# Performance work log

Measured on AMD Instinct MI355X. Metric: run time of the kernel, lower is better.

## Reference

```python
import jax, jax.numpy as jnp
import numpy as np
from jax import lax

R = 3
D = (2 * R + 1) ** 2  # 49 local offsets


def _unfold(x, r):
    # torch F.unfold(kernel=2r+1, padding=r): (B,C,H,W) -> (B, C*K*K, H, W),
    # channel-major (c, ky, kx) ordering, matching conv_general_dilated_patches.
    k = 2 * r + 1
    return lax.conv_general_dilated_patches(
        x, (k, k), (1, 1), [(r, r), (r, r)],
        dimension_numbers=("NCHW", "OIHW", "NCHW"))


def _l2norm(x, eps=1e-12):
    n = jnp.sqrt(jnp.sum(x * x, axis=1, keepdims=True))
    return x / jnp.maximum(n, eps)


def setup_inputs() -> dict:
    key = jax.random.key(0)
    ks = jax.random.split(key, 8)
    B, Cin, Cmid, H, W = 2, 256, 128, 112, 112
    phi_cur = jax.random.normal(ks[0], (B, Cin, H, W), jnp.float32)
    phi_rnd = jax.random.normal(ks[1], (B, Cin, H, W), jnp.float32)
    P_cur = jax.random.normal(ks[2], (B, 3, H, W), jnp.float32)
    P_rnd = jax.random.normal(ks[3], (B, 3, H, W), jnp.float32)
    Wq = jax.random.normal(ks[4], (Cmid, Cin), jnp.float32) * 0.05
    Wk = jax.random.normal(ks[5], (Cmid, Cin), jnp.float32) * 0.05
    Wv = jax.random.normal(ks[6], (D, D), jnp.float32) * 0.1
    bv = jnp.zeros((D,), jnp.float32)
    gamma = jnp.array(1.0, jnp.float32)
    return dict(phi_cur=phi_cur, phi_rnd=phi_rnd, P_cur=P_cur, P_rnd=P_rnd,
                Wq=Wq, Wk=Wk, Wv=Wv, bv=bv, gamma=gamma)


def reference(phi_cur, phi_rnd, P_cur, P_rnd, Wq, Wk, Wv, bv, gamma):
    B, _, H, W = phi_cur.shape
    # 1x1 convs + channel L2 normalize
    q = _l2norm(jnp.einsum('oc,bchw->bohw', Wq, phi_cur))
    k = _l2norm(jnp.einsum('oc,bchw->bohw', Wk, phi_rnd))
    # local cost volume: patches (B, Cmid, D, H, W)
    patches = _unfold(k, R).reshape(B, -1, D, H, W)
    corr = jnp.einsum('bchw,bcdhw->bdhw', q, patches)  # (B,D,H,W)
    vol_corr = jnp.einsum('ed,bdhw->behw', Wv, corr) + bv[None, :, None, None]
    # geometric bias
    Pr = _unfold(P_rnd, R).reshape(B, 3, D, H, W)
    dP = P_cur[:, :, None, :, :] - Pr  # (B,3,D,H,W)
    dz = dP[:, 2]
    dist = jnp.sqrt(jnp.clip(jnp.sum(dP * dP, axis=1), 1e-12, None))
    logits = vol_corr + gamma * (-dist - 0.5 * jnp.abs(dz))
    w = jax.nn.softmax(logits, axis=1)
    off = jnp.arange(-R, R + 1, dtype=w.dtype)
    dY, dX = jnp.meshgrid(off, off, indexing='ij')
    offx = dX.reshape(1, D, 1, 1)
    offy = dY.reshape(1, D, 1, 1)
    du = jnp.sum(w * offx, axis=1, keepdims=True)
    dv = jnp.sum(w * offy, axis=1, keepdims=True)
    conf = jnp.max(w, axis=1, keepdims=True)
    return du, dv, conf
```

## Files before the change

kernel.cpp:

```cpp
#include <hip/hip_runtime.h>
#include <hip/hip_bf16.h>
#include <math.h>

constexpr int B    = 2;
constexpr int CIN  = 256;
constexpr int CMID = 128;
constexpr int H    = 112;
constexpr int W    = 112;
constexpr int HW   = H * W;
constexpr int NPIX = B * HW;
constexpr int RAD  = 3;
constexpr int KS   = 7;
constexpr int DD   = 49;

typedef __attribute__((ext_vector_type(8))) short  short8;
typedef __attribute__((ext_vector_type(4))) float  float4v;

__device__ __forceinline__ unsigned pkbf(float a, float b) {
    union { __hip_bfloat162 h; unsigned u; } c;
    c.h = __float22bfloat162_rn(make_float2(a, b));
    return c.u;
}

constexpr int PSTR = 264;

__global__ __launch_bounds__(256) void proj_mfma(
    const float* __restrict__ phi_cur, const float* __restrict__ phi_rnd,
    const float* __restrict__ Wq, const float* __restrict__ Wk,
    unsigned short* __restrict__ q_ws, unsigned short* __restrict__ k_ws)
{
    __shared__ unsigned short pt[64 * PSTR];
    __shared__ float red[4][64];

    const int tid  = threadIdx.x;
    const int lane = tid & 63;
    const int wv   = __builtin_amdgcn_readfirstlane(tid >> 6);
    const int t    = blockIdx.y;

    const float* __restrict__ phi = t ? phi_rnd : phi_cur;
    const float* __restrict__ Wm  = t ? Wk : Wq;
    unsigned short* __restrict__ outp = t ? k_ws : q_ws;

    const int pgb = blockIdx.x * 64;
    const int b   = pgb / HW;
    const int pim = pgb % HW;
    const float* pbase = phi + (size_t)b * CIN * HW + pim;

#pragma unroll
    for (int pass = 0; pass < 8; ++pass) {
        const int idx = pass * 256 + tid;
        const int cp  = idx >> 4;
        const int pq  = idx & 15;
        const int c0  = cp * 2;
        const float4 va = *(const float4*)(pbase + (size_t)c0 * HW + pq * 4);
        const float4 vb = *(const float4*)(pbase + (size_t)(c0 + 1) * HW + pq * 4);
        *(unsigned*)(pt + (pq * 4 + 0) * PSTR + c0) = pkbf(va.x, vb.x);
        *(unsigned*)(pt + (pq * 4 + 1) * PSTR + c0) = pkbf(va.y, vb.y);
        *(unsigned*)(pt + (pq * 4 + 2) * PSTR + c0) = pkbf(va.z, vb.z);
        *(unsigned*)(pt + (pq * 4 + 3) * PSTR + c0) = pkbf(va.w, vb.w);
    }

    const int m = lane & 15, quad = lane >> 4;
    short8 af[2][8];
#pragma unroll
    for (int ot = 0; ot < 2; ++ot)
#pragma unroll
        for (int kc = 0; kc < 8; ++kc) {
            const float* wr = Wm + (size_t)(wv * 32 + ot * 16 + m) * CIN
                                 + kc * 32 + quad * 8;
            const float4 w0 = *(const float4*)(wr);
            const float4 w1 = *(const float4*)(wr + 4);
            union { short8 s; unsigned u[4]; } pk;
            pk.u[0] = pkbf(w0.x, w0.y);
            pk.u[1] = pkbf(w0.z, w0.w);
            pk.u[2] = pkbf(w1.x, w1.y);
            pk.u[3] = pkbf(w1.z, w1.w);
            af[ot][kc] = pk.s;
        }

    __syncthreads();

    float4v acc[2][4];
#pragma unroll
    for (int ot = 0; ot < 2; ++ot)
#pragma unroll
        for (int nt = 0; nt < 4; ++nt) acc[ot][nt] = (float4v)0.f;

#pragma unroll
    for (int kc = 0; kc < 8; ++kc) {
        short8 bf[4];
#pragma unroll
        for (int nt = 0; nt < 4; ++nt)
            bf[nt] = *(const short8*)(pt + (nt * 16 + m) * PSTR + kc * 32 + quad * 8);
#pragma unroll
        for (int ot = 0; ot < 2; ++ot)
#pragma unroll
            for (int nt = 0; nt < 4; ++nt)
                acc[ot][nt] = __builtin_amdgcn_mfma_f32_16x16x32_bf16(
                    af[ot][kc], bf[nt], acc[ot][nt], 0, 0, 0);
    }

#pragma unroll
    for (int nt = 0; nt < 4; ++nt) {
        float ss = 0.f;
#pragma unroll
        for (int ot = 0; ot < 2; ++ot)
#pragma unroll
            for (int r = 0; r < 4; ++r)
                ss = fmaf(acc[ot][nt][r], acc[ot][nt][r], ss);
        ss += __shfl_xor(ss, 16, 64);
        ss += __shfl_xor(ss, 32, 64);
        if (quad == 0) red[wv][nt * 16 + m] = ss;
    }
    __syncthreads();

    float inv[4];
#pragma unroll
    for (int nt = 0; nt < 4; ++nt) {
        const int px = nt * 16 + m;
        const float tot = red[0][px] + red[1][px] + red[2][px] + red[3][px];
        inv[nt] = 1.f / fmaxf(sqrtf(tot), 1e-12f);
    }

#pragma unroll
    for (int nt = 0; nt < 4; ++nt)
#pragma unroll
        for (int ot = 0; ot < 2; ++ot) {
            uint2 st;
            st.x = pkbf(acc[ot][nt][0] * inv[nt], acc[ot][nt][1] * inv[nt]);
            st.y = pkbf(acc[ot][nt][2] * inv[nt], acc[ot][nt][3] * inv[nt]);
            *(uint2*)(outp + (size_t)(pgb + nt * 16 + m) * CMID
                      + wv * 32 + ot * 16 + quad * 4) = st;
        }
}

constexpr int TILE = 16;
constexpr int COLS = TILE + 6;
constexpr int NV   = KS * COLS;

__global__ __launch_bounds__(256, 4) void corr_kernel(
    const unsigned short* __restrict__ q_ws, const unsigned short* __restrict__ k_ws,
    const float* __restrict__ P_cur, const float* __restrict__ P_rnd,
    const float* __restrict__ Wvm, const float* __restrict__ bv,
    const float* __restrict__ gamma_p, float* __restrict__ out)
{
    __shared__ float cs[TILE][52];
    __shared__ float prt[3 * NV];

    const int tid  = threadIdx.x;
    const int lane = tid & 63;
    const int wv   = __builtin_amdgcn_readfirstlane(tid >> 6);
    const int w0   = blockIdx.x * TILE;
    const int h    = blockIdx.y;
    const int b    = blockIdx.z;

#pragma unroll
    for (int pass = 0; pass < 2; ++pass) {
        const int idx = pass * 256 + tid;
        if (idx < 3 * NV) {
            const int ch = idx / NV;
            const int vi = idx % NV;
            const int rr = vi / COLS;
            const int cc = vi % COLS;
            const int hh = h + rr - RAD;
            const int ww = w0 + cc - RAD;
            float v = 0.f;
            if (hh >= 0 && hh < H && ww >= 0 && ww < W)
                v = P_rnd[((size_t)b * 3 + ch) * HW + hh * W + ww];
            prt[idx] = v;
        }
    }

    if (tid < TILE * 3)
        cs[tid / 3][49 + tid % 3] = 0.f;

    const int  ld    = (lane < DD) ? lane : 0;
    const bool valid = (lane < DD);
    float wrow[52];
#pragma unroll
    for (int e = 0; e < DD; ++e) wrow[e] = Wvm[ld * DD + e];
    wrow[49] = wrow[50] = wrow[51] = 0.f;
    const float bvv   = bv[ld];
    const float gamma = gamma_p[0];

    const int m = lane & 15, quad = lane >> 4;
    const unsigned short* qbase =
        q_ws + (size_t)(b * HW + h * W + w0 + m) * CMID + quad * 8;

    for (int g = wv; g < 14; g += 4) {
        const int r  = g >> 1;
        const int nt = g & 1;
        const int hh = h + r - RAD;
        const int ww = w0 + nt * 16 + m - RAD;
        const bool inb = (hh >= 0) && (hh < H) && (ww >= 0) && (ww < W);
        const unsigned short* kbase =
            k_ws + (size_t)(b * HW + hh * W + ww) * CMID + quad * 8;

        float4v acc = (float4v)0.f;
#pragma unroll
        for (int kc = 0; kc < 4; ++kc) {
            const short8 afrag = *(const short8*)(qbase + kc * 32);
            const short8 bfrag = inb ? *(const short8*)(kbase + kc * 32)
                                     : (short8)0;
            acc = __builtin_amdgcn_mfma_f32_16x16x32_bf16(afrag, bfrag, acc, 0, 0, 0);
        }
#pragma unroll
        for (int reg = 0; reg < 4; ++reg) {
            const int p   = quad * 4 + reg;
            const int off = nt * 16 + m - p;
            if (off >= 0 && off <= 6)
                cs[p][r * 7 + off] = acc[reg];
        }
    }
    __syncthreads();

    const int dyr = ld / KS;
    const int dxc = ld % KS;
    const int dy  = dyr - RAD;
    const int dx  = dxc - RAD;
    const float fdx = (float)dx, fdy = (float)dy;

    for (int i = 0; i < 4; ++i) {
        const int pl = wv * 4 + i;
        const int pg = b * HW + h * W + w0 + pl;

        const int vi = dyr * COLS + pl + dxc;
        const float rx = prt[vi];
        const float ry = prt[NV + vi];
        const float rz = prt[2 * NV + vi];
        const float* pc = P_cur + (size_t)b * 3 * HW + (h * W + w0 + pl);
        const float cx = pc[0], cy = pc[HW], cz = pc[2 * HW];
        const float dpx = cx - rx, dpy = cy - ry, dpz = cz - rz;
        const float dist = sqrtf(fmaxf(dpx * dpx + dpy * dpy + dpz * dpz, 1e-12f));

        float logit = -INFINITY;
        if (valid) {
            float v = bvv;
#pragma unroll
            for (int e4 = 0; e4 < 13; ++e4) {
                const float4 c4 = *(const float4*)&cs[pl][e4 * 4];
                v = fmaf(wrow[e4 * 4 + 0], c4.x, v);
                v = fmaf(wrow[e4 * 4 + 1], c4.y, v);
                v = fmaf(wrow[e4 * 4 + 2], c4.z, v);
                v = fmaf(wrow[e4 * 4 + 3], c4.w, v);
            }
            logit = v + gamma * (-dist - 0.5f * fabsf(dpz));
        }

        float lmax = logit;
#pragma unroll
        for (int off = 32; off; off >>= 1)
            lmax = fmaxf(lmax, __shfl_xor(lmax, off, 64));
        const float e1 = valid ? __expf(logit - lmax) : 0.f;

        float s0 = e1, s1 = e1 * fdx, s2 = e1 * fdy;
#pragma unroll
        for (int off = 32; off; off >>= 1) {
            s0 += __shfl_xor(s0, off, 64);
            s1 += __shfl_xor(s1, off, 64);
            s2 += __shfl_xor(s2, off, 64);
        }

        if (lane == 0) {
            const float rZ = 1.f / s0;
            out[pg]            = s1 * rZ;
            out[NPIX + pg]     = s2 * rZ;
            out[2 * NPIX + pg] = rZ;
        }
    }
}

extern "C" void kernel_launch(void* const* d_in, const int* in_sizes, int n_in,
                              void* d_out, int out_size, void* d_ws, size_t ws_size,
                              hipStream_t stream)
{
    const float* phi_cur = (const float*)d_in[0];
    const float* phi_rnd = (const float*)d_in[1];
    const float* P_cur   = (const float*)d_in[2];
    const float* P_rnd   = (const float*)d_in[3];
    const float* Wq      = (const float*)d_in[4];
    const float* Wk      = (const float*)d_in[5];
    const float* Wv      = (const float*)d_in[6];
    const float* bv      = (const float*)d_in[7];
    const float* gm      = (const float*)d_in[8];
    float* out = (float*)d_out;

    unsigned short* ws   = (unsigned short*)d_ws;
    unsigned short* q_ws = ws;
    unsigned short* k_ws = q_ws + (size_t)NPIX * CMID;

    proj_mfma<<<dim3(NPIX / 64, 2), 256, 0, stream>>>(
        phi_cur, phi_rnd, Wq, Wk, q_ws, k_ws);

    corr_kernel<<<dim3(W / TILE, H, B), 256, 0, stream>>>(
        q_ws, k_ws, P_cur, P_rnd, Wv, bv, gm, out);
}
```

Before: 148.0 us.

## Map one pixel per lane with online softmax over a 4x16 tile

The correlation kernel now handles a 4x16 pixel tile per block, so grid blocks drop fourfold and the P_rnd halo is shared across four rows. In the epilogue each lane owns one pixel: it loads all 49 correlations into registers and loops over offsets with an online softmax. Wv rows are read as wave-uniform scalar loads, which removes the cross-lane shuffle reductions and the idle lanes 49-63. The cost is a serial 49x49 FMA loop per lane plus two exps per offset, and higher register pressure from the 49-element array.

```diff
diff --git a/kernel.cpp b/kernel.cpp
--- a/kernel.cpp
+++ b/kernel.cpp
@@ -134,9 +134,12 @@
         }
 }
 
-constexpr int TILE = 16;
-constexpr int COLS = TILE + 6;
-constexpr int NV   = KS * COLS;
+constexpr int BH   = 4;
+constexpr int BW   = 16;
+constexpr int PRH  = BH + 6;
+constexpr int PRW  = BW + 6;
+constexpr int PRN  = PRH * PRW;
+constexpr int CSTR = 53;
 
 __global__ __launch_bounds__(256, 4) void corr_kernel(
     const unsigned short* __restrict__ q_ws, const unsigned short* __restrict__ k_ws,
@@ -144,25 +147,25 @@
     const float* __restrict__ Wvm, const float* __restrict__ bv,
     const float* __restrict__ gamma_p, float* __restrict__ out)
 {
-    __shared__ float cs[TILE][52];
-    __shared__ float prt[3 * NV];
+    __shared__ float cs[64 * CSTR];
+    __shared__ float prt[3 * PRN];
 
     const int tid  = threadIdx.x;
     const int lane = tid & 63;
     const int wv   = __builtin_amdgcn_readfirstlane(tid >> 6);
-    const int w0   = blockIdx.x * TILE;
-    const int h    = blockIdx.y;
+    const int w0   = blockIdx.x * BW;
+    const int h0   = blockIdx.y * BH;
     const int b    = blockIdx.z;
 
 #pragma unroll
-    for (int pass = 0; pass < 2; ++pass) {
+    for (int pass = 0; pass < 3; ++pass) {
         const int idx = pass * 256 + tid;
-        if (idx < 3 * NV) {
-            const int ch = idx / NV;
-            const int vi = idx % NV;
-            const int rr = vi / COLS;
-            const int cc = vi % COLS;
-            const int hh = h + rr - RAD;
+        if (idx < 3 * PRN) {
+            const int ch = idx / PRN;
+            const int sl = idx % PRN;
+            const int rr = sl / PRW;
+            const int cc = sl % PRW;
+            const int hh = h0 + rr - RAD;
             const int ww = w0 + cc - RAD;
             float v = 0.f;
             if (hh >= 0 && hh < H && ww >= 0 && ww < W)
@@ -171,28 +174,17 @@
         }
     }
 
-    if (tid < TILE * 3)
-        cs[tid / 3][49 + tid % 3] = 0.f;
-
-    const int  ld    = (lane < DD) ? lane : 0;
-    const bool valid = (lane < DD);
-    float wrow[52];
-#pragma unroll
-    for (int e = 0; e < DD; ++e) wrow[e] = Wvm[ld * DD + e];
-    wrow[49] = wrow[50] = wrow[51] = 0.f;
-    const float bvv   = bv[ld];
-    const float gamma = gamma_p[0];
-
     const int m = lane & 15, quad = lane >> 4;
-    const unsigned short* qbase =
-        q_ws + (size_t)(b * HW + h * W + w0 + m) * CMID + quad * 8;
-
-    for (int g = wv; g < 14; g += 4) {
-        const int r  = g >> 1;
-        const int nt = g & 1;
-        const int hh = h + r - RAD;
+    for (int g = wv; g < 56; g += 4) {
+        const int hq = g / 14;
+        const int rem = g % 14;
+        const int r  = rem >> 1;
+        const int nt = rem & 1;
+        const int hh = h0 + hq + r - RAD;
         const int ww = w0 + nt * 16 + m - RAD;
         const bool inb = (hh >= 0) && (hh < H) && (ww >= 0) && (ww < W);
+        const unsigned short* qbase =
+            q_ws + (size_t)(b * HW + (h0 + hq) * W + w0 + m) * CMID + quad * 8;
         const unsigned short* kbase =
             k_ws + (size_t)(b * HW + hh * W + ww) * CMID + quad * 8;
 
@@ -209,65 +201,59 @@
             const int p   = quad * 4 + reg;
             const int off = nt * 16 + m - p;
             if (off >= 0 && off <= 6)
-                cs[p][r * 7 + off] = acc[reg];
+                cs[(hq * 16 + p) * CSTR + r * 7 + off] = acc[reg];
         }
     }
     __syncthreads();
 
-    const int dyr = ld / KS;
-    const int dxc = ld % KS;
-    const int dy  = dyr - RAD;
-    const int dx  = dxc - RAD;
-    const float fdx = (float)dx, fdy = (float)dy;
-
-    for (int i = 0; i < 4; ++i) {
-        const int pl = wv * 4 + i;
-        const int pg = b * HW + h * W + w0 + pl;
-
-        const int vi = dyr * COLS + pl + dxc;
+    const int hq = lane >> 4;
+    const int pq = lane & 15;
+    const int h  = h0 + hq;
+    const int w  = w0 + pq;
+    const int pg = b * HW + h * W + w;
+
+    float cr[DD];
+#pragma unroll
+    for (int e = 0; e < DD; ++e) cr[e] = cs[lane * CSTR + e];
+
+    const float* pc = P_cur + (size_t)b * 3 * HW + h * W + w;
+    const float cx = pc[0], cy = pc[HW], cz = pc[2 * HW];
+    const float gamma = gamma_p[0];
+
+    float m_run = -INFINITY, s0 = 0.f, s1 = 0.f, s2 = 0.f;
+    int dyr = 0, dxc = 0;
+    for (int d = 0; d < DD; ++d) {
+        const int du = __builtin_amdgcn_readfirstlane(d);
+        const float* wrow = Wvm + du * DD;
+        float lg = bv[du];
+#pragma unroll
+        for (int e = 0; e < DD; ++e)
+            lg = fmaf(wrow[e], cr[e], lg);
+
+        const int vi = (hq + dyr) * PRW + pq + dxc;
         const float rx = prt[vi];
-        const float ry = prt[NV + vi];
-        const float rz = prt[2 * NV + vi];
-        const float* pc = P_cur + (size_t)b * 3 * HW + (h * W + w0 + pl);
-        const float cx = pc[0], cy = pc[HW], cz = pc[2 * HW];
+        const float ry = prt[PRN + vi];
+        const float rz = prt[2 * PRN + vi];
         const float dpx = cx - rx, dpy = cy - ry, dpz = cz - rz;
         const float dist = sqrtf(fmaxf(dpx * dpx + dpy * dpy + dpz * dpz, 1e-12f));
-
-        float logit = -INFINITY;
-        if (valid) {
-            float v = bvv;
-#pragma unroll
-            for (int e4 = 0; e4 < 13; ++e4) {
-                const float4 c4 = *(const float4*)&cs[pl][e4 * 4];
-                v = fmaf(wrow[e4 * 4 + 0], c4.x, v);
-                v = fmaf(wrow[e4 * 4 + 1], c4.y, v);
-                v = fmaf(wrow[e4 * 4 + 2], c4.z, v);
-                v = fmaf(wrow[e4 * 4 + 3], c4.w, v);
-            }
-            logit = v + gamma * (-dist - 0.5f * fabsf(dpz));
-        }
-
-        float lmax = logit;
-#pragma unroll
-        for (int off = 32; off; off >>= 1)
-            lmax = fmaxf(lmax, __shfl_xor(lmax, off, 64));
-        const float e1 = valid ? __expf(logit - lmax) : 0.f;
-
-        float s0 = e1, s1 = e1 * fdx, s2 = e1 * fdy;
-#pragma unroll
-        for (int off = 32; off; off >>= 1) {
-            s0 += __shfl_xor(s0, off, 64);
-            s1 += __shfl_xor(s1, off, 64);
-            s2 += __shfl_xor(s2, off, 64);
-        }
-
-        if (lane == 0) {
-            const float rZ = 1.f / s0;
-            out[pg]            = s1 * rZ;
-            out[NPIX + pg]     = s2 * rZ;
-            out[2 * NPIX + pg] = rZ;
-        }
-    }
+        lg += gamma * (-dist - 0.5f * fabsf(dpz));
+
+        const float fdx = (float)(dxc - RAD), fdy = (float)(dyr - RAD);
+        const float nm = fmaxf(m_run, lg);
+        const float sc = __expf(m_run - nm);
+        const float e1 = __expf(lg - nm);
+        s0 = fmaf(s0, sc, e1);
+        s1 = fmaf(s1, sc, e1 * fdx);
+        s2 = fmaf(s2, sc, e1 * fdy);
+        m_run = nm;
+
+        if (++dxc == KS) { dxc = 0; ++dyr; }
+    }
+
+    const float rZ = 1.f / s0;
+    out[pg]            = s1 * rZ;
+    out[NPIX + pg]     = s2 * rZ;
+    out[2 * NPIX + pg] = rZ;
 }
 
 extern "C" void kernel_launch(void* const* d_in, const int* in_sizes, int n_in,
@@ -292,6 +278,6 @@
     proj_mfma<<<dim3(NPIX / 64, 2), 256, 0, stream>>>(
         phi_cur, phi_rnd, Wq, Wk, q_ws, k_ws);
 
-    corr_kernel<<<dim3(W / TILE, H, B), 256, 0, stream>>>(
+    corr_kernel<<<dim3(W / BW, H / BH, B), 256, 0, stream>>>(
         q_ws, k_ws, P_cur, P_rnd, Wv, bv, gm, out);
 }
```

New measurement: 165.4 us. 1.12x slower.
